# Kernel tuning notes

Hardware: AMD Instinct MI355X
Metric: run time of the kernel (lower is better)

Reference implementation:

```python
import jax, jax.numpy as jnp
import numpy as np

N_QUBITS = 4
DIM = 2 ** N_QUBITS  # 16-dim statevector
KERNEL = 3
STRIDE = 1
PADDING = 1


def _rot_mats(w):
    # PennyLane Rot(phi, theta, omega) = RZ(omega) RY(theta) RZ(phi)
    phi, theta, omega = w[:, 0], w[:, 1], w[:, 2]
    c = jnp.cos(theta / 2)
    s = jnp.sin(theta / 2)
    em = jnp.exp(-0.5j * (phi + omega))
    ep = jnp.exp(0.5j * (phi + omega))
    ed = jnp.exp(0.5j * (phi - omega))
    edm = jnp.exp(-0.5j * (phi - omega))
    row0 = jnp.stack([em * c, -ed * s], axis=-1)
    row1 = jnp.stack([edm * s, ep * c], axis=-1)
    return jnp.stack([row0, row1], axis=-2)  # [n_qubits, 2, 2]


def _apply_1q(state, U, wire):
    # state: [M] + [2]*n, wire axis is 1+wire (wire 0 is most significant)
    s = jnp.moveaxis(state, 1 + wire, -1)
    s = jnp.einsum('...b,ab->...a', s, U)
    return jnp.moveaxis(s, -1, 1 + wire)


def _apply_cnot(state, c, t):
    s = jnp.moveaxis(state, (1 + c, 1 + t), (-2, -1))
    shp = s.shape
    s = s.reshape(shp[:-2] + (4,))[..., jnp.array([0, 1, 3, 2])].reshape(shp)
    return jnp.moveaxis(s, (-2, -1), (1 + c, 1 + t))


def _forward(x, W_pre, b_pre, W_post, b_post, q_weights):
    B, C, L = x.shape
    xp = jnp.pad(x, ((0, 0), (0, 0), (PADDING, PADDING)))
    L_out = (L + 2 * PADDING - KERNEL) // STRIDE + 1
    starts = jnp.arange(L_out) * STRIDE
    # windows: [B, C, L_out, K] -> flatten channel-major like torch reshape
    win = xp[:, :, starts[:, None] + jnp.arange(KERNEL)[None, :]]
    win = win.transpose(0, 2, 1, 3).reshape(B, L_out, C * KERNEL)
    pre = win @ W_pre.T + b_pre  # [B, L_out, n_qubits]
    # AmplitudeEmbedding: pad to 2**n and normalize
    v = jnp.pad(pre, ((0, 0), (0, 0), (0, DIM - N_QUBITS)))
    v = v / jnp.linalg.norm(v, axis=-1, keepdims=True)
    state = v.reshape(B * L_out, *([2] * N_QUBITS)).astype(jnp.complex64)
    U = _rot_mats(q_weights)
    for i in range(N_QUBITS):
        state = _apply_1q(state, U[i], i)
    for i in range(N_QUBITS - 1):
        state = _apply_cnot(state, i, i + 1)
    flat = state.reshape(B * L_out, DIM)
    probs = jnp.real(flat) ** 2 + jnp.imag(flat) ** 2
    # PauliZ expectation per wire: sign of bit i (wire 0 = MSB)
    bits = (jnp.arange(DIM)[None, :] >> (N_QUBITS - 1 - jnp.arange(N_QUBITS)[:, None])) & 1
    z = (1 - 2 * bits).astype(probs.dtype)  # [n_qubits, DIM]
    expz = (probs @ z.T).reshape(B, L_out, N_QUBITS)
    out = expz @ W_post.T + b_post  # [B, L_out, out_channels]
    return out.transpose(0, 2, 1)


def setup_inputs() -> dict:
    key = jax.random.key(0)
    ks = jax.random.split(key, 6)
    B, C, L = 32, 80, 3000
    OUT = 512
    return {
        'x': jax.random.normal(ks[0], (B, C, L), dtype=jnp.float32),
        'W_pre': jax.random.normal(ks[1], (N_QUBITS, C * KERNEL), dtype=jnp.float32) * 0.06,
        'b_pre': jax.random.normal(ks[2], (N_QUBITS,), dtype=jnp.float32) * 0.06,
        'W_post': jax.random.normal(ks[3], (OUT, N_QUBITS), dtype=jnp.float32) * 0.4,
        'b_post': jax.random.normal(ks[4], (OUT,), dtype=jnp.float32) * 0.4,
        'q_weights': jax.random.normal(ks[5], (N_QUBITS, 3), dtype=jnp.float32),
    }


def reference(x, W_pre, b_pre, W_post, b_post, q_weights):
    return _forward(x, W_pre, b_pre, W_post, b_post, q_weights)
```

## Files before the change

kernel.cpp:

```cpp
#include <hip/hip_runtime.h>
#include <math.h>

#define C_IN 80
#define L_IN 3000
#define OUT_C 512
#define TL1 128
#define NT1 256
#define NT2 256

typedef float floatx4 __attribute__((ext_vector_type(4)));

struct c2f { float x, y; };

__device__ __forceinline__ c2f cmul(c2f a, c2f b) {
    return { a.x*b.x - a.y*b.y, a.x*b.y + a.y*b.x };
}
__device__ __forceinline__ c2f csel(c2f a, c2f b, int bit) {
    c2f r; r.x = bit ? b.x : a.x; r.y = bit ? b.y : a.y; return r;
}
__device__ __forceinline__ float quadform(const float4* __restrict__ A, float4 p) {
    float4 r0 = A[0], r1 = A[1], r2 = A[2], r3 = A[3];
    return p.x*(r0.x*p.x + r0.y*p.y + r0.z*p.z + r0.w*p.w)
         + p.y*(r1.x*p.x + r1.y*p.y + r1.z*p.z + r1.w*p.w)
         + p.z*(r2.x*p.x + r2.y*p.y + r2.z*p.z + r2.w*p.w)
         + p.w*(r3.x*p.x + r3.y*p.y + r3.z*p.z + r3.w*p.w);
}

__global__ __launch_bounds__(NT1) void qconv_expz_kernel(
    const float* __restrict__ x,
    const float* __restrict__ W_pre,
    const float* __restrict__ b_pre,
    const float* __restrict__ qw,
    float4* __restrict__ expz)
{
    __shared__ float4 s_wpre[C_IN*3];
    __shared__ float4 s_A[16];
    __shared__ float4 s_part[TL1];

    const int t  = threadIdx.x;
    const int b  = blockIdx.y;
    const int l0 = blockIdx.x * TL1;

    for (int i = t; i < C_IN*3; i += NT1) {
        s_wpre[i] = make_float4(W_pre[0*C_IN*3 + i], W_pre[1*C_IN*3 + i],
                                W_pre[2*C_IN*3 + i], W_pre[3*C_IN*3 + i]);
    }
    __syncthreads();

    if (t < 64) {
        c2f U[4][2][2];
        #pragma unroll
        for (int i = 0; i < 4; ++i) {
            float phi = qw[i*3+0], theta = qw[i*3+1], omega = qw[i*3+2];
            float sh, ch;  sincosf(0.5f*theta, &sh, &ch);
            float s1, c1;  sincosf(0.5f*(phi+omega), &s1, &c1);
            float s2, cv;  sincosf(0.5f*(phi-omega), &s2, &cv);
            U[i][0][0] = {  c1*ch, -s1*ch };
            U[i][0][1] = { -cv*sh, -s2*sh };
            U[i][1][0] = {  cv*sh, -s2*sh };
            U[i][1][1] = {  c1*ch,  s1*ch };
        }
        const int q  = t >> 4;
        const int j  = (t >> 2) & 3;
        const int jp = t & 3;
        const int j2  = (j  >> 1) & 1, j3  = j  & 1;
        const int jp2 = (jp >> 1) & 1, jp3 = jp & 1;
        float s = 0.f;
        #pragma unroll
        for (int k = 0; k < 16; ++k) {
            int m = k ^ ((k >> 1) & 1);
            m ^= ((m >> 2) & 1) << 1;
            m ^= ((m >> 3) & 1) << 2;
            const int m0 = (m >> 3) & 1, m1 = (m >> 2) & 1;
            const int m2 = (m >> 1) & 1, m3 = m & 1;
            c2f w01 = cmul(U[0][m0][0], U[1][m1][0]);
            c2f av = cmul(w01, cmul(csel(U[2][m2][0], U[2][m2][1], j2),
                                    csel(U[3][m3][0], U[3][m3][1], j3)));
            c2f bv = cmul(w01, cmul(csel(U[2][m2][0], U[2][m2][1], jp2),
                                    csel(U[3][m3][0], U[3][m3][1], jp3)));
            float z = 1.f - 2.f * ((k >> (3 - q)) & 1);
            s += z * (av.x*bv.x + av.y*bv.y);
        }
        ((float*)s_A)[t] = s;
    }

    const int i = t & (TL1 - 1);
    const int h = t >> 7;
    const int l = l0 + i;
    const bool lvalid = (l < L_IN);

    float4 acc = (h == 0) ? make_float4(b_pre[0], b_pre[1], b_pre[2], b_pre[3])
                          : make_float4(0.f, 0.f, 0.f, 0.f);
    if (lvalid) {
        const float* __restrict__ xrow = x + (size_t)b * C_IN * L_IN + (size_t)(h*40) * L_IN + l;
        const bool has_m1 = (l >= 1);
        const bool has_p1 = (l + 1 < L_IN);
        #pragma unroll 4
        for (int c = 0; c < 40; ++c) {
            const float* r = xrow + c * L_IN;
            float xa = has_m1 ? r[-1] : 0.f;
            float xb = r[0];
            float xc = has_p1 ? r[1] : 0.f;
            float4 w0 = s_wpre[(h*40+c)*3+0], w1 = s_wpre[(h*40+c)*3+1], w2 = s_wpre[(h*40+c)*3+2];
            acc.x += w0.x*xa + w1.x*xb + w2.x*xc;
            acc.y += w0.y*xa + w1.y*xb + w2.y*xc;
            acc.z += w0.z*xa + w1.z*xb + w2.z*xc;
            acc.w += w0.w*xa + w1.w*xb + w2.w*xc;
        }
    }
    if (h == 1) s_part[i] = acc;
    __syncthreads();

    if (t < TL1 && lvalid) {
        float4 p = acc;
        float4 q2 = s_part[t];
        p.x += q2.x; p.y += q2.y; p.z += q2.z; p.w += q2.w;
        const float inv = 1.f / (p.x*p.x + p.y*p.y + p.z*p.z + p.w*p.w);
        float4 e;
        e.x = quadform(&s_A[0],  p) * inv;
        e.y = quadform(&s_A[4],  p) * inv;
        e.z = quadform(&s_A[8],  p) * inv;
        e.w = quadform(&s_A[12], p) * inv;
        expz[(size_t)b * L_IN + l] = e;
    }
}

__global__ __launch_bounds__(NT2) void expand_kernel(
    const float4* __restrict__ expz,
    const float* __restrict__ W_post,
    const float* __restrict__ b_post,
    float* __restrict__ out)
{
    __shared__ float4 s_e[L_IN];

    const int t    = threadIdx.x;
    const int og   = blockIdx.x;
    const int b    = blockIdx.y;
    const int w    = t >> 6;
    const int lane = t & 63;

    const float4* ep = expz + (size_t)b * L_IN;
    for (int i = t; i < L_IN; i += NT2) s_e[i] = ep[i];

    const int obase = og*32 + w*8;
    float4 wv[8]; float bb[8];
    #pragma unroll
    for (int r = 0; r < 8; ++r) {
        wv[r] = *reinterpret_cast<const float4*>(&W_post[(obase + r) * 4]);
        bb[r] = b_post[obase + r];
    }
    __syncthreads();

    float* orow = out + ((size_t)b * OUT_C + obase) * L_IN;
    #pragma unroll 2
    for (int it = 0; it < (L_IN + 255) / 256; ++it) {
        const int l = it*256 + lane*4;
        if (l < L_IN) {
            const float4 e0 = s_e[l+0];
            const float4 e1 = s_e[l+1];
            const float4 e2 = s_e[l+2];
            const float4 e3 = s_e[l+3];
            #pragma unroll
            for (int r = 0; r < 8; ++r) {
                floatx4 st;
                st.x = wv[r].x*e0.x + wv[r].y*e0.y + wv[r].z*e0.z + wv[r].w*e0.w + bb[r];
                st.y = wv[r].x*e1.x + wv[r].y*e1.y + wv[r].z*e1.z + wv[r].w*e1.w + bb[r];
                st.z = wv[r].x*e2.x + wv[r].y*e2.y + wv[r].z*e2.z + wv[r].w*e2.w + bb[r];
                st.w = wv[r].x*e3.x + wv[r].y*e3.y + wv[r].z*e3.z + wv[r].w*e3.w + bb[r];
                *reinterpret_cast<floatx4*>(orow + (size_t)r * L_IN + l) = st;
            }
        }
    }
}

extern "C" void kernel_launch(void* const* d_in, const int* in_sizes, int n_in,
                              void* d_out, int out_size, void* d_ws, size_t ws_size,
                              hipStream_t stream) {
    const float* x      = (const float*)d_in[0];
    const float* W_pre  = (const float*)d_in[1];
    const float* b_pre  = (const float*)d_in[2];
    const float* W_post = (const float*)d_in[3];
    const float* b_post = (const float*)d_in[4];
    const float* qw     = (const float*)d_in[5];
    float* out = (float*)d_out;
    float4* expz = (float4*)d_ws;

    const int B = in_sizes[0] / (C_IN * L_IN);
    dim3 grid1((L_IN + TL1 - 1) / TL1, B);
    qconv_expz_kernel<<<grid1, NT1, 0, stream>>>(x, W_pre, b_pre, qw, expz);
    dim3 grid2(OUT_C / 32, B);
    expand_kernel<<<grid2, NT2, 0, stream>>>(expz, W_post, b_post, out);
}
```

Baseline: 50.37 us.

## Restructure expand kernel with SoA shared layout and register-cached expz halves

The expz values are stored in shared memory as four separate component arrays instead of float4, and the block size doubles to 512 threads, with each wave handling 4 output channels instead of 8. Each wave loads a half-row (1500 positions) of expz into registers once and reuses it across its 4 output channels. The aim is to cut shared-memory read traffic and bank conflicts per output and to get more waves issuing stores. The kernel is dominated by output stores, so the gain may be limited, and register pressure goes up.

```diff
diff --git a/kernel.cpp b/kernel.cpp
--- a/kernel.cpp
+++ b/kernel.cpp
@@ -6,7 +6,8 @@
 #define OUT_C 512
 #define TL1 128
 #define NT1 256
-#define NT2 256
+#define NT2 512
+#define HALF 1500
 
 typedef float floatx4 __attribute__((ext_vector_type(4)));
 
@@ -131,7 +132,10 @@
     const float* __restrict__ b_post,
     float* __restrict__ out)
 {
-    __shared__ float4 s_e[L_IN];
+    __shared__ float s_ex[L_IN];
+    __shared__ float s_ey[L_IN];
+    __shared__ float s_ez[L_IN];
+    __shared__ float s_ew[L_IN];
 
     const int t    = threadIdx.x;
     const int og   = blockIdx.x;
@@ -140,34 +144,53 @@
     const int lane = t & 63;
 
     const float4* ep = expz + (size_t)b * L_IN;
-    for (int i = t; i < L_IN; i += NT2) s_e[i] = ep[i];
-
-    const int obase = og*32 + w*8;
-    float4 wv[8]; float bb[8];
+    for (int i = t; i < L_IN; i += NT2) {
+        float4 v = ep[i];
+        s_ex[i] = v.x; s_ey[i] = v.y; s_ez[i] = v.z; s_ew[i] = v.w;
+    }
+
+    const int obase = og*32 + w*4;
+    float4 wv[4]; float bb[4];
     #pragma unroll
-    for (int r = 0; r < 8; ++r) {
+    for (int r = 0; r < 4; ++r) {
         wv[r] = *reinterpret_cast<const float4*>(&W_post[(obase + r) * 4]);
         bb[r] = b_post[obase + r];
     }
     __syncthreads();
 
-    float* orow = out + ((size_t)b * OUT_C + obase) * L_IN;
-    #pragma unroll 2
-    for (int it = 0; it < (L_IN + 255) / 256; ++it) {
-        const int l = it*256 + lane*4;
-        if (l < L_IN) {
-            const float4 e0 = s_e[l+0];
-            const float4 e1 = s_e[l+1];
-            const float4 e2 = s_e[l+2];
-            const float4 e3 = s_e[l+3];
+    #pragma unroll
+    for (int half = 0; half < 2; ++half) {
+        const int base = half * HALF;
+        float4 ex[6], ey[6], ez[6], ew[6];
+        #pragma unroll
+        for (int it = 0; it < 6; ++it) {
+            const int ll = it*256 + lane*4;
+            if (ll < HALF) {
+                const int l = base + ll;
+                ex[it] = *reinterpret_cast<const float4*>(&s_ex[l]);
+                ey[it] = *reinterpret_cast<const float4*>(&s_ey[l]);
+                ez[it] = *reinterpret_cast<const float4*>(&s_ez[l]);
+                ew[it] = *reinterpret_cast<const float4*>(&s_ew[l]);
+            } else {
+                ex[it] = ey[it] = ez[it] = ew[it] = make_float4(0.f,0.f,0.f,0.f);
+            }
+        }
+        #pragma unroll
+        for (int r = 0; r < 4; ++r) {
+            float* orow = out + ((size_t)b * OUT_C + obase + r) * L_IN + base;
+            const float4 wr = wv[r];
+            const float  br = bb[r];
             #pragma unroll
-            for (int r = 0; r < 8; ++r) {
-                floatx4 st;
-                st.x = wv[r].x*e0.x + wv[r].y*e0.y + wv[r].z*e0.z + wv[r].w*e0.w + bb[r];
-                st.y = wv[r].x*e1.x + wv[r].y*e1.y + wv[r].z*e1.z + wv[r].w*e1.w + bb[r];
-                st.z = wv[r].x*e2.x + wv[r].y*e2.y + wv[r].z*e2.z + wv[r].w*e2.w + bb[r];
-                st.w = wv[r].x*e3.x + wv[r].y*e3.y + wv[r].z*e3.z + wv[r].w*e3.w + bb[r];
-                *reinterpret_cast<floatx4*>(orow + (size_t)r * L_IN + l) = st;
+            for (int it = 0; it < 6; ++it) {
+                const int ll = it*256 + lane*4;
+                if (ll < HALF) {
+                    floatx4 st;
+                    st.x = wr.x*ex[it].x + wr.y*ey[it].x + wr.z*ez[it].x + wr.w*ew[it].x + br;
+                    st.y = wr.x*ex[it].y + wr.y*ey[it].y + wr.z*ez[it].y + wr.w*ew[it].y + br;
+                    st.z = wr.x*ex[it].z + wr.y*ey[it].z + wr.z*ez[it].z + wr.w*ew[it].z + br;
+                    st.w = wr.x*ex[it].w + wr.y*ey[it].w + wr.z*ez[it].w + wr.w*ew[it].w + br;
+                    *reinterpret_cast<floatx4*>(orow + ll) = st;
+                }
             }
         }
     }
```

Result: no change. 49.83 us (-1.1%).
